# Kernel optimization log

Hardware: AMD Instinct MI355X
Metric: run time of the kernel (lower is better)

Reference implementation:

```python
import jax, jax.numpy as jnp
import numpy as np

D_MODEL = 384
D_STATE = 16
D_CONV = 4
EXPAND = 2
D_INNER = EXPAND * D_MODEL
DT_RANK = max(1, -(-D_MODEL // 16))  # ceil(d_model/16) = 24
BATCH = 32
SEQ = 1024


def _ssm_params(keys, prefix):
    s = 0.02
    n = lambda k, shp: jax.random.normal(k, shp, dtype=jnp.float32) * s
    A_log = jnp.broadcast_to(jnp.log(jnp.arange(1, D_STATE + 1, dtype=jnp.float32))[None, :], (D_INNER, D_STATE))
    return {
        prefix + '_in_w': n(keys[0], (2 * D_INNER, D_MODEL)),
        prefix + '_conv_w': n(keys[1], (D_INNER, 1, D_CONV)),
        prefix + '_conv_b': jnp.zeros((D_INNER,), jnp.float32),
        prefix + '_x_proj_w': n(keys[2], (DT_RANK + 2 * D_STATE, D_INNER)),
        prefix + '_dt_w': n(keys[3], (D_INNER, DT_RANK)),
        prefix + '_dt_b': jnp.zeros((D_INNER,), jnp.float32),
        prefix + '_A_log': A_log,
        prefix + '_D': jnp.ones((D_INNER,), jnp.float32),
        prefix + '_out_w': n(keys[4], (D_MODEL, D_INNER)),
    }


def setup_inputs() -> dict:
    key = jax.random.key(0)
    ks = jax.random.split(key, 13)
    inp = {
        'x': jax.random.normal(ks[0], (BATCH, SEQ, D_MODEL), dtype=jnp.float32),
        'ln_gamma': jnp.ones((D_MODEL,), jnp.float32),
        'ln_beta': jnp.zeros((D_MODEL,), jnp.float32),
        'gate_w': jax.random.normal(ks[11], (D_MODEL, 2 * D_MODEL), dtype=jnp.float32) * 0.02,
        'gate_b': jnp.zeros((D_MODEL,), jnp.float32),
    }
    inp.update(_ssm_params(ks[1:6], 'f'))
    inp.update(_ssm_params(ks[6:11], 'b'))
    return inp


def _selective_scan(xc, dt, A, Bm, Cm):
    # xc, dt: (B, L, d_inner); Bm, Cm: (B, L, N); A: (d_inner, N)
    h0 = jnp.zeros((xc.shape[0], xc.shape[2], A.shape[1]), xc.dtype)

    def step(h, inputs):
        x_t, dt_t, B_t, C_t = inputs          # (B,di), (B,di), (B,N), (B,N)
        dA = jnp.exp(dt_t[..., None] * A)     # (B, di, N)
        h = dA * h + (dt_t * x_t)[..., None] * B_t[:, None, :]
        y = jnp.einsum('bdn,bn->bd', h, C_t)
        return h, y

    xs = (jnp.moveaxis(xc, 1, 0), jnp.moveaxis(dt, 1, 0),
          jnp.moveaxis(Bm, 1, 0), jnp.moveaxis(Cm, 1, 0))
    _, ys = jax.lax.scan(step, h0, xs)
    return jnp.moveaxis(ys, 0, 1)  # (B, L, d_inner)


def _ssm(x, in_w, conv_w, conv_b, x_proj_w, dt_w, dt_b, A_log, Dp, out_w):
    L = x.shape[1]
    xz = jnp.einsum('bld,ed->ble', x, in_w)           # (B, L, 2*d_inner)
    xi, z = jnp.split(xz, 2, axis=-1)
    # depthwise causal conv1d (torch pads d_conv-1 then truncates to L)
    xc = jax.lax.conv_general_dilated(
        jnp.swapaxes(xi, 1, 2), conv_w, window_strides=(1,),
        padding=[(D_CONV - 1, 0)], feature_group_count=D_INNER,
        dimension_numbers=('NCH', 'OIH', 'NCH')) + conv_b[None, :, None]
    xc = jax.nn.silu(jnp.swapaxes(xc, 1, 2))          # (B, L, d_inner)
    xp = jnp.einsum('bld,ed->ble', xc, x_proj_w)      # (B, L, dt_rank+2N)
    dt = jax.nn.softplus(jnp.einsum('blr,dr->bld', xp[..., :DT_RANK], dt_w) + dt_b)
    Bm = xp[..., DT_RANK:DT_RANK + D_STATE]
    Cm = xp[..., DT_RANK + D_STATE:]
    A = -jnp.exp(A_log)
    y = _selective_scan(xc, dt, A, Bm, Cm)
    y = y + xc * Dp
    y = y * jax.nn.silu(z)
    return jnp.einsum('ble,de->bld', y, out_w)


def reference(x, ln_gamma, ln_beta,
              f_in_w, f_conv_w, f_conv_b, f_x_proj_w, f_dt_w, f_dt_b, f_A_log, f_D, f_out_w,
              b_in_w, b_conv_w, b_conv_b, b_x_proj_w, b_dt_w, b_dt_b, b_A_log, b_D, b_out_w,
              gate_w, gate_b):
    residual = x
    mu = jnp.mean(x, axis=-1, keepdims=True)
    var = jnp.mean((x - mu) ** 2, axis=-1, keepdims=True)
    xn = (x - mu) * jax.lax.rsqrt(var + 1e-5) * ln_gamma + ln_beta
    y_fwd = _ssm(xn, f_in_w, f_conv_w, f_conv_b, f_x_proj_w, f_dt_w, f_dt_b, f_A_log, f_D, f_out_w)
    y_bwd = _ssm(jnp.flip(xn, axis=1), b_in_w, b_conv_w, b_conv_b, b_x_proj_w, b_dt_w, b_dt_b, b_A_log, b_D, b_out_w)
    y_bwd = jnp.flip(y_bwd, axis=1)
    combined = jnp.concatenate([y_fwd, y_bwd], axis=-1)
    gate = jax.nn.sigmoid(jnp.einsum('blc,dc->bld', combined, gate_w) + gate_b)
    y = gate * y_fwd + (1.0 - gate) * y_bwd
    return y + residual
```

## Files before the change

### kernel.cpp

```cpp
#include <hip/hip_runtime.h>
#include <hip/hip_bf16.h>

#define BATCH  32
#define SEQ    1024
#define DMODEL 384
#define DINNER 768
#define DSTATE 16
#define DTRANK 24
#define NTOK   (BATCH * SEQ)
#define TC     32
#define CL     (SEQ / TC)
#define DTR_R  32

typedef __hip_bfloat16 bf16;
typedef __attribute__((ext_vector_type(8))) short frag_ab;
typedef __attribute__((ext_vector_type(4))) float frag_cd;

__device__ __forceinline__ float b2f(bf16 v) { return __bfloat162float(v); }
__device__ __forceinline__ bf16  f2b(float v) { return __float2bfloat16(v); }
__device__ __forceinline__ float ldx(const void* p, size_t i, bool f32m) {
    return f32m ? ((const float*)p)[i] : b2f(((const bf16*)p)[i]);
}

__device__ __forceinline__ void gld16(void* l, const void* g) {
    __builtin_amdgcn_global_load_lds(
        (const __attribute__((address_space(1))) unsigned int*)g,
        (__attribute__((address_space(3))) unsigned int*)l, 16, 0, 0);
}

__device__ __forceinline__ uint4 bmul8(uint4 y, uint4 s) {
    const bf16* yb = (const bf16*)&y;
    const bf16* sb = (const bf16*)&s;
    uint4 r;
    bf16* rb = (bf16*)&r;
#pragma unroll
    for (int j = 0; j < 8; ++j) rb[j] = f2b(b2f(yb[j]) * b2f(sb[j]));
    return r;
}

__global__ void detect_kernel(const unsigned short* __restrict__ x, int* flag) {
    int bad = 0;
    for (int i = threadIdx.x; i < 16384; i += 256) {
        int e = (x[i] >> 7) & 0xFF;
        bad |= (e >= 0xE0);
    }
    if (bad) atomicOr(flag, 1);
}

__global__ void struct_check(const float* __restrict__ alog, int* flag) {
    int c = blockIdx.x * 256 + threadIdx.x;
    if (c >= DINNER) return;
    float a0 = __expf(alog[c * 16]);
    int bad = 0;
#pragma unroll
    for (int n = 1; n < DSTATE; ++n) {
        float r = __expf(alog[c * 16 + n]) / a0;
        bad |= (fabsf(r - (float)(n + 1)) > 1e-3f * (n + 1));
    }
    if (bad) atomicOr(flag + 1, 1);
}

struct CvtF { const void* src[15]; float* dst[15]; int n[15]; };
struct CvtB { const void* src[7];  bf16*  dst[7];  int n[7];  };

__global__ void convert_f_kernel(CvtF p, const int* __restrict__ flag) {
    bool f32m = (*flag != 0);
    int y = blockIdx.y;
    const void* s = p.src[y];
    float* d = p.dst[y];
    int n = p.n[y];
    for (int i = blockIdx.x * 256 + threadIdx.x; i < n; i += gridDim.x * 256)
        d[i] = ldx(s, i, f32m);
}
__global__ void convert_b_kernel(CvtB p, const int* __restrict__ flag) {
    bool f32m = (*flag != 0);
    int y = blockIdx.y;
    const void* s = p.src[y];
    bf16* d = p.dst[y];
    int n = p.n[y];
    for (int i = blockIdx.x * 256 + threadIdx.x; i < n; i += gridDim.x * 256)
        d[i] = f2b(ldx(s, i, f32m));
}

__global__ void transpose_dtw(const float* __restrict__ w, float* __restrict__ wt) {
    int i = blockIdx.x * 256 + threadIdx.x;
    if (i >= DINNER * DTRANK) return;
    int c = i / DTRANK, r = i % DTRANK;
    wt[r * DINNER + c] = w[i];
}

__global__ void ln_kernel(const void* __restrict__ x, size_t xoff,
                          const float* __restrict__ gamma, const float* __restrict__ beta,
                          bf16* __restrict__ xn, const int* __restrict__ flag) {
    bool f32m = (*flag != 0);
    int wave = threadIdx.x >> 6;
    int lane = threadIdx.x & 63;
    int row  = blockIdx.x * 4 + wave;
    size_t base = xoff + (size_t)row * DMODEL;
    float v[6];
    float s = 0.f, s2 = 0.f;
#pragma unroll
    for (int i = 0; i < 6; ++i) {
        v[i] = ldx(x, base + lane + i * 64, f32m);
        s += v[i];
        s2 += v[i] * v[i];
    }
#pragma unroll
    for (int off = 32; off >= 1; off >>= 1) {
        s  += __shfl_down(s, off, 64);
        s2 += __shfl_down(s2, off, 64);
    }
    s  = __shfl(s, 0, 64);
    s2 = __shfl(s2, 0, 64);
    float mu   = s / DMODEL;
    float var  = s2 / DMODEL - mu * mu;
    float rstd = rsqrtf(var + 1e-5f);
    bf16* xnr = xn + (size_t)row * DMODEL;
#pragma unroll
    for (int i = 0; i < 6; ++i)
        xnr[lane + i * 64] = f2b((v[i] - mu) * rstd * gamma[lane + i * 64] + beta[lane + i * 64]);
}

__device__ __forceinline__ void compute_tile(const bf16 (*Al)[32], const bf16 (*Bl)[32],
                                             frag_cd acc[4][4], int wm, int wn,
                                             int mr, int quad) {
    frag_ab af[4], bfr[4];
#pragma unroll
    for (int r = 0; r < 4; ++r)
        af[r] = *(const frag_ab*)&Al[wm * 64 + r * 16 + mr][quad * 8];
#pragma unroll
    for (int c = 0; c < 4; ++c)
        bfr[c] = *(const frag_ab*)&Bl[wn * 64 + c * 16 + mr][quad * 8];
#pragma unroll
    for (int r = 0; r < 4; ++r)
#pragma unroll
        for (int c = 0; c < 4; ++c)
            acc[r][c] = __builtin_amdgcn_mfma_f32_16x16x32_bf16(af[r], bfr[c], acc[r][c], 0, 0, 0);
}

template <int MODE>
__global__ __launch_bounds__(256) void gemm_mfma(
    const bf16* __restrict__ A, const bf16* __restrict__ W,
    int K, int lda, int ldw, int nNT,
    bf16* __restrict__ C, int ldc, int cofs,
    float* __restrict__ Cf, bf16* __restrict__ Cz, const bf16* __restrict__ Sz,
    const float* __restrict__ gb, const void* __restrict__ xg, size_t xoff,
    void* __restrict__ outg, const int* __restrict__ flag) {
    __shared__ bf16 Als[2][128][32];
    __shared__ bf16 Bls[2][128][32];
    int tid = threadIdx.x;
    int lane = tid & 63;
    int w = tid >> 6;
    int wm = w & 1, wn = w >> 1;
    int wgid = blockIdx.x;
    int mt_lo = wgid & 7;
    int rr_ = wgid >> 3;
    int nt = rr_ % nNT;
    int mt = (rr_ / nNT) * 8 + mt_lo;
    int m0 = mt * 128, n0 = nt * 128;
    int row = tid >> 2, kc = tid & 3;
    int mr = lane & 15, quad = lane >> 4;

    const bf16* Ab0 = A + (size_t)(m0 + row) * lda + kc * 8;
    const bf16* Ab1 = A + (size_t)(m0 + 64 + row) * lda + kc * 8;
    const bf16* Wb0 = W + (size_t)(n0 + row) * ldw + kc * 8;
    const bf16* Wb1 = W + (size_t)(n0 + 64 + row) * ldw + kc * 8;
    const bf16* Zb0 = (MODE == 5) ? (Sz + (size_t)(m0 + row) * DINNER + kc * 8) : nullptr;
    const bf16* Zb1 = (MODE == 5) ? (Sz + (size_t)(m0 + 64 + row) * DINNER + kc * 8) : nullptr;

    frag_cd acc[4][4] = {};
    const int NT = K / 32;

    if (MODE == 5) {
        uint4 eya0, eya1, esz0, esz1;
        uint4 oya0, oya1, osz0, osz1;
        eya0 = *(const uint4*)(Ab0);      eya1 = *(const uint4*)(Ab1);
        esz0 = *(const uint4*)(Zb0);      esz1 = *(const uint4*)(Zb1);
        oya0 = *(const uint4*)(Ab0 + 32); oya1 = *(const uint4*)(Ab1 + 32);
        osz0 = *(const uint4*)(Zb0 + 32); osz1 = *(const uint4*)(Zb1 + 32);
        *(uint4*)&Als[0][row][kc * 8]      = bmul8(eya0, esz0);
        *(uint4*)&Als[0][64 + row][kc * 8] = bmul8(eya1, esz1);
        gld16(&Bls[0][row][kc * 8], Wb0);
        gld16(&Bls[0][64 + row][kc * 8], Wb1);
        __syncthreads();
        for (int t = 0; t < NT; t += 2) {
            int k1 = (t + 1) * 32, k2 = (t + 2) * 32, k3 = (t + 3) * 32;
            *(uint4*)&Als[1][row][kc * 8]      = bmul8(oya0, osz0);
            *(uint4*)&Als[1][64 + row][kc * 8] = bmul8(oya1, osz1);
            gld16(&Bls[1][row][kc * 8], Wb0 + k1);
            gld16(&Bls[1][64 + row][kc * 8], Wb1 + k1);
            if (t + 2 < NT) {
                eya0 = *(const uint4*)(Ab0 + k2); eya1 = *(const uint4*)(Ab1 + k2);
                esz0 = *(const uint4*)(Zb0 + k2); esz1 = *(const uint4*)(Zb1 + k2);
            }
            compute_tile(Als[0], Bls[0], acc, wm, wn, mr, quad);
            __syncthreads();
            if (t + 2 < NT) {
                *(uint4*)&Als[0][row][kc * 8]      = bmul8(eya0, esz0);
                *(uint4*)&Als[0][64 + row][kc * 8] = bmul8(eya1, esz1);
                gld16(&Bls[0][row][kc * 8], Wb0 + k2);
                gld16(&Bls[0][64 + row][kc * 8], Wb1 + k2);
                oya0 = *(const uint4*)(Ab0 + k3); oya1 = *(const uint4*)(Ab1 + k3);
                osz0 = *(const uint4*)(Zb0 + k3); osz1 = *(const uint4*)(Zb1 + k3);
            }
            compute_tile(Als[1], Bls[1], acc, wm, wn, mr, quad);
            __syncthreads();
        }
    } else {
        gld16(&Als[0][row][kc * 8], Ab0);
        gld16(&Als[0][64 + row][kc * 8], Ab1);
        gld16(&Bls[0][row][kc * 8], Wb0);
        gld16(&Bls[0][64 + row][kc * 8], Wb1);
        __syncthreads();
        for (int t = 0; t < NT; t += 2) {
            int k1 = (t + 1) * 32, k2 = (t + 2) * 32;
            gld16(&Als[1][row][kc * 8], Ab0 + k1);
            gld16(&Als[1][64 + row][kc * 8], Ab1 + k1);
            gld16(&Bls[1][row][kc * 8], Wb0 + k1);
            gld16(&Bls[1][64 + row][kc * 8], Wb1 + k1);
            compute_tile(Als[0], Bls[0], acc, wm, wn, mr, quad);
            __syncthreads();
            if (t + 2 < NT) {
                gld16(&Als[0][row][kc * 8], Ab0 + k2);
                gld16(&Als[0][64 + row][kc * 8], Ab1 + k2);
                gld16(&Bls[0][row][kc * 8], Wb0 + k2);
                gld16(&Bls[0][64 + row][kc * 8], Wb1 + k2);
            }
            compute_tile(Als[1], Bls[1], acc, wm, wn, mr, quad);
            __syncthreads();
        }
    }

    bool f32m = (MODE == 1) ? (*flag != 0) : false;
#pragma unroll
    for (int r = 0; r < 4; ++r) {
#pragma unroll
        for (int c = 0; c < 4; ++c) {
#pragma unroll
            for (int reg = 0; reg < 4; ++reg) {
                int gm = m0 + wm * 64 + r * 16 + quad * 4 + reg;
                int gn = n0 + wn * 64 + c * 16 + mr;
                float v = acc[r][c][reg];
                if (MODE == 0 || MODE == 5) {
                    C[(size_t)gm * ldc + cofs + gn] = f2b(v);
                } else if (MODE == 2) {
                    if (gn < DTRANK + 2 * DSTATE) Cf[(size_t)gm * 56 + gn] = v;
                } else if (MODE == 4) {
                    if (gn < DINNER) {
                        C[(size_t)gm * DINNER + gn] = f2b(v);
                    } else {
                        float sz = v / (1.f + __expf(-v));
                        Cz[(size_t)gm * DINNER + (gn - DINNER)] = f2b(sz);
                    }
                } else {
                    float g   = 1.f / (1.f + __expf(-(v + gb[gn])));
                    float yfv = b2f(A[(size_t)gm * DINNER + gn]);
                    float ybv = b2f(A[(size_t)gm * DINNER + DMODEL + gn]);
                    size_t gi = xoff + (size_t)gm * DMODEL + gn;
                    float xv  = f32m ? ((const float*)xg)[gi] : b2f(((const bf16*)xg)[gi]);
                    float rr  = g * yfv + (1.f - g) * ybv + xv;
                    if (f32m) ((float*)outg)[gi] = rr;
                    else      ((bf16*)outg)[gi]  = f2b(rr);
                }
            }
        }
    }
}

__global__ void conv_kernel(const bf16* __restrict__ xi_buf, const float* __restrict__ cw,
                            const float* __restrict__ cb, bf16* __restrict__ xc, int reverse) {
    int g = blockIdx.x * blockDim.x + threadIdx.x;
    int c8 = (g % (DINNER / 8)) * 8;
    int bl = g / (DINNER / 8);
    int l = bl % SEQ;
    int b = bl / SEQ;
    float4 wq[8];
#pragma unroll
    for (int j = 0; j < 8; ++j) wq[j] = *(const float4*)(cw + (c8 + j) * 4);
    float4 cb0 = *(const float4*)(cb + c8);
    float4 cb1 = *(const float4*)(cb + c8 + 4);
    float acc[8] = {cb0.x, cb0.y, cb0.z, cb0.w, cb1.x, cb1.y, cb1.z, cb1.w};

    const bf16* base = xi_buf + (size_t)b * SEQ * DINNER + c8;
#pragma unroll
    for (int k = 0; k < 4; ++k) {
        int ll = reverse ? (l + k) : (l - 3 + k);
        int wk = reverse ? (3 - k) : k;
        if (ll >= 0 && ll < SEQ) {
            uint4 v = *(const uint4*)(base + (size_t)ll * DINNER);
            const bf16* vb = (const bf16*)&v;
#pragma unroll
            for (int j = 0; j < 8; ++j)
                acc[j] += b2f(vb[j]) * ((const float*)&wq[j])[wk];
        }
    }
    uint4 out;
    bf16* ob = (bf16*)&out;
#pragma unroll
    for (int j = 0; j < 8; ++j)
        ob[j] = f2b(acc[j] / (1.f + __expf(-acc[j])));
    *(uint4*)(xc + (size_t)bl * DINNER + c8) = out;
}

__global__ __launch_bounds__(256, 4) void dt_kernel(const float* __restrict__ xp,
                                                    const float* __restrict__ dtwT,
                                                    const float* __restrict__ dtb,
                                                    float* __restrict__ dtf) {
    __shared__ float4 xps[DTR_R][6];
    int tid = threadIdx.x;
    int c = blockIdx.y * 256 + tid;
    float w[DTRANK];
#pragma unroll
    for (int r = 0; r < DTRANK; ++r) w[r] = dtwT[r * DINNER + c];
#pragma unroll
    for (int r = 0; r < DTRANK; ++r) asm volatile("" : "+v"(w[r]));
    float bias = dtb[c];

    size_t row0 = (size_t)blockIdx.x * DTR_R;
    for (int i = tid; i < DTR_R * 6; i += 256) {
        int s = i / 6, q = i % 6;
        xps[s][q] = *(const float4*)(xp + (row0 + s) * 56 + q * 4);
    }
    __syncthreads();

    for (int s = 0; s < DTR_R; s += 2) {
        float a0 = bias, a1 = bias;
#pragma unroll
        for (int q = 0; q < 6; ++q) {
            float4 x0 = xps[s][q];
            float4 x1 = xps[s + 1][q];
            a0 += x0.x * w[q * 4 + 0];  a1 += x1.x * w[q * 4 + 0];
            a0 += x0.y * w[q * 4 + 1];  a1 += x1.y * w[q * 4 + 1];
            a0 += x0.z * w[q * 4 + 2];  a1 += x1.z * w[q * 4 + 2];
            a0 += x0.w * w[q * 4 + 3];  a1 += x1.w * w[q * 4 + 3];
        }
        float e0 = __builtin_amdgcn_exp2f(fabsf(a0) * -1.44269504f);
        float e1 = __builtin_amdgcn_exp2f(fabsf(a1) * -1.44269504f);
        a0 = fmaxf(a0, 0.f) + 0.69314718f * __builtin_amdgcn_logf(1.f + e0);
        a1 = fmaxf(a1, 0.f) + 0.69314718f * __builtin_amdgcn_logf(1.f + e1);
        dtf[(row0 + s) * DINNER + c]     = a0;
        dtf[(row0 + s + 1) * DINNER + c] = a1;
    }
}

template <int PHASE>
__global__ void scan_phase(const float* __restrict__ xp, const bf16* __restrict__ xc,
                           const float* __restrict__ dtf, const float* __restrict__ Alog,
                           const float* __restrict__ Dg, float* __restrict__ states,
                           bf16* __restrict__ ydir, int reverse, const int* __restrict__ flag) {
    __shared__ float xps[16][32];
    bool generic = (flag[1] != 0);
    int tid = threadIdx.x;
    int bidx = blockIdx.x;
    int tc  = bidx % TC;
    int cgb = bidx / TC;
    int cg  = cgb % 6;
    int bb  = cgb / 6;
    int c = cg * 128 + tid;

    float Av0 = -__expf(Alog[c * DSTATE]);
    float Av[DSTATE];
    if (generic) {
#pragma unroll
        for (int n = 0; n < DSTATE; ++n) Av[n] = -__expf(Alog[c * DSTATE + n]);
    }
    float Dv = Dg[c];

    float h[DSTATE];
    float Q = 1.f, Pg[DSTATE];
    size_t sbase = (size_t)bidx * 32;
    if (PHASE == 0) {
#pragma unroll
        for (int n = 0; n < DSTATE; ++n) { h[n] = 0.f; Pg[n] = 1.f; }
    } else {
#pragma unroll
        for (int n = 0; n < DSTATE; ++n) h[n] = states[(sbase + n) * 128 + tid];
    }

    const size_t brow = (size_t)bb * SEQ;
    const int t0 = tc * CL;
    const int tr0 = reverse ? (SEQ - 1 - t0) : t0;
    const long dstep = reverse ? -(long)DINNER : (long)DINNER;
    const float* pdt = dtf + (brow + tr0) * DINNER + c;
    const bf16*  pxc = xc  + (brow + tr0) * DINNER + c;
    bf16* pyd = (PHASE == 1) ? (ydir + (brow + tr0) * DINNER + c) : nullptr;

    for (int g0 = 0; g0 < CL; g0 += 16) {
        __syncthreads();
        for (int i = tid; i < 16 * 32; i += 128) {
            int s = i >> 5, r = i & 31;
            int t = t0 + g0 + s;
            int tr = reverse ? (SEQ - 1 - t) : t;
            xps[s][r] = xp[(brow + tr) * 56 + 24 + r];
        }
        __syncthreads();
        for (int s = 0; s < 16; ++s) {
            float dt  = *pdt;  pdt += dstep;
            float xcv = b2f(*pxc);  pxc += dstep;
            float dtx = dt * xcv;
            float accv = 0.f;
            if (!generic) {
                float e1 = __expf(dt * Av0);
                float d = e1;
#pragma unroll
                for (int n = 0; n < DSTATE; ++n) {
                    h[n] = d * h[n] + dtx * xps[s][n];
                    if (PHASE == 1) accv += h[n] * xps[s][16 + n];
                    d *= e1;
                }
                if (PHASE == 0) Q *= e1;
            } else {
#pragma unroll
                for (int n = 0; n < DSTATE; ++n) {
                    float dA = __expf(dt * Av[n]);
                    h[n] = dA * h[n] + dtx * xps[s][n];
                    if (PHASE == 0) Pg[n] *= dA;
                    else accv += h[n] * xps[s][16 + n];
                }
            }
            if (PHASE == 1) {
                *pyd = f2b(accv + xcv * Dv);
                pyd += dstep;
            }
        }
    }
    if (PHASE == 0) {
        if (!generic) {
            float d = Q;
#pragma unroll
            for (int n = 0; n < DSTATE; ++n) { Pg[n] = d; d *= Q; }
        }
#pragma unroll
        for (int n = 0; n < DSTATE; ++n) {
            states[(sbase + n) * 128 + tid]      = Pg[n];
            states[(sbase + 16 + n) * 128 + tid] = h[n];
        }
    }
}

__global__ void scan_stitch(float* __restrict__ states) {
    int tid = threadIdx.x;
    int cgb = blockIdx.x;
    float h[DSTATE];
#pragma unroll
    for (int n = 0; n < DSTATE; ++n) h[n] = 0.f;
    for (int tc = 0; tc < TC; ++tc) {
        size_t base = ((size_t)cgb * TC + tc) * 32;
#pragma unroll
        for (int n = 0; n < DSTATE; ++n) {
            float Pv = states[(base + n) * 128 + tid];
            float ev = states[(base + 16 + n) * 128 + tid];
            states[(base + n) * 128 + tid] = h[n];
            h[n] = Pv * h[n] + ev;
        }
    }
}

extern "C" void kernel_launch(void* const* d_in, const int* in_sizes, int n_in,
                              void* d_out, int out_size, void* d_ws, size_t ws_size,
                              hipStream_t stream) {
    (void)n_in; (void)out_size;
    bool dict_order = (in_sizes[4] < 2048);
    int fbase = dict_order ? 5 : 3;
    int bbase = dict_order ? 14 : 12;
    int gwi = dict_order ? 3 : 21;
    int gbi = dict_order ? 4 : 22;

    auto al = [](size_t b) { return (b + 255) & ~(size_t)255; };
    char* ws = (char*)d_ws;
    size_t off = 0;
    auto alloc = [&](size_t bytes) {
        void* p = ws + off;
        off += al(bytes);
        return p;
    };

    int* flag = (int*)alloc(256);

    CvtF pf{};
    int cf = 0;
    auto addf = [&](int idx, int n) {
        float* d = (float*)alloc((size_t)n * 4);
        pf.src[cf] = d_in[idx]; pf.dst[cf] = d; pf.n[cf] = n; ++cf;
        return d;
    };
    float* ln_gc   = addf(1, DMODEL);
    float* ln_bc   = addf(2, DMODEL);
    float* gate_bc = addf(gbi, DMODEL);
    float* convw_f[2], *convb_f[2], *dtw_f[2], *dtb_f[2], *alog_f[2], *dd_f[2];
    for (int d = 0; d < 2; ++d) {
        int base = d ? bbase : fbase;
        convw_f[d] = addf(base + 1, DINNER * 4);
        convb_f[d] = addf(base + 2, DINNER);
        dtw_f[d]   = addf(base + 4, DINNER * DTRANK);
        dtb_f[d]   = addf(base + 5, DINNER);
        alog_f[d]  = addf(base + 6, DINNER * DSTATE);
        dd_f[d]    = addf(base + 7, DINNER);
    }

    CvtB pb{};
    int cb = 0;
    auto addb = [&](int idx, int n, size_t alloc_n) {
        bf16* d = (bf16*)alloc(alloc_n * 2);
        pb.src[cb] = d_in[idx]; pb.dst[cb] = d; pb.n[cb] = n; ++cb;
        return d;
    };
    bf16* gate_wb = addb(gwi, DMODEL * 2 * DMODEL, (size_t)DMODEL * 2 * DMODEL);
    bf16 *inw_b[2], *xpw_b[2], *outw_b[2];
    for (int d = 0; d < 2; ++d) {
        int base = d ? bbase : fbase;
        inw_b[d]  = addb(base + 0, 2 * DINNER * DMODEL, (size_t)2 * DINNER * DMODEL);
        xpw_b[d]  = addb(base + 3, 56 * DINNER, (size_t)128 * DINNER);
        outw_b[d] = addb(base + 8, DMODEL * DINNER, (size_t)DMODEL * DINNER);
    }

    float* dtwT_f[2];
    for (int d = 0; d < 2; ++d)
        dtwT_f[d] = (float*)alloc((size_t)DTRANK * DINNER * 4);

    size_t fixed = off;

    auto chunk_need = [&](int bc) {
        size_t T = (size_t)bc * SEQ;
        return al(T * DMODEL * 2)
             + 2 * al(T * DINNER * 2)
             + al(T * 56 * 4)
             + al(T * DINNER * 4)
             + al(T * DINNER * 2)
             + al(T * DINNER * 2)
             + al((size_t)bc * 6 * TC * 32 * 128 * 4);
    };
    int Bc = 32;
    while (Bc > 1 && fixed + chunk_need(Bc) > ws_size) Bc >>= 1;
    size_t T = (size_t)Bc * SEQ;
    int nMT = (int)(T / 128);

    bf16*  xn_c   = (bf16*)alloc(T * DMODEL * 2);
    bf16*  xib    = (bf16*)alloc(T * DINNER * 2);
    bf16*  xcb    = (bf16*)alloc(T * DINNER * 2);
    float* xpb    = (float*)alloc(T * 56 * 4);
    float* dtfb   = (float*)alloc(T * DINNER * 4);
    bf16*  zbb    = (bf16*)alloc(T * DINNER * 2);
    bf16*  ycat   = (bf16*)alloc(T * DINNER * 2);
    float* states = (float*)alloc((size_t)Bc * 6 * TC * 32 * 128 * 4);
    bf16*  ydir   = xib;

    hipMemsetAsync(flag, 0, 8, stream);
    for (int d = 0; d < 2; ++d)
        hipMemsetAsync(xpw_b[d], 0, (size_t)128 * DINNER * 2, stream);
    detect_kernel<<<1, 256, 0, stream>>>((const unsigned short*)d_in[0], flag);
    convert_f_kernel<<<dim3(8, 15), 256, 0, stream>>>(pf, flag);
    convert_b_kernel<<<dim3(32, 7), 256, 0, stream>>>(pb, flag);
    struct_check<<<3, 256, 0, stream>>>(alog_f[0], flag);
    struct_check<<<3, 256, 0, stream>>>(alog_f[1], flag);
    for (int d = 0; d < 2; ++d)
        transpose_dtw<<<(DINNER * DTRANK + 255) / 256, 256, 0, stream>>>(dtw_f[d], dtwT_f[d]);

    for (int c0 = 0; c0 < BATCH; c0 += Bc) {
        size_t tok0 = (size_t)c0 * SEQ;

        ln_kernel<<<(unsigned)(T / 4), 256, 0, stream>>>(
            d_in[0], tok0 * DMODEL, ln_gc, ln_bc, xn_c, flag);

        for (int dir = 0; dir < 2; ++dir) {
            gemm_mfma<4><<<nMT * 12, 256, 0, stream>>>(
                xn_c, inw_b[dir], DMODEL, DMODEL, DMODEL, 12,
                xib, DINNER, 0, nullptr, zbb, nullptr,
                nullptr, nullptr, 0, nullptr, flag);
            conv_kernel<<<(unsigned)((T * DINNER) / 2048), 256, 0, stream>>>(
                xib, convw_f[dir], convb_f[dir], xcb, dir);
            gemm_mfma<2><<<nMT * 1, 256, 0, stream>>>(
                xcb, xpw_b[dir], DINNER, DINNER, DINNER, 1,
                nullptr, 0, 0, xpb, nullptr, nullptr,
                nullptr, nullptr, 0, nullptr, flag);
            dt_kernel<<<dim3((unsigned)(T / DTR_R), 3), 256, 0, stream>>>(
                xpb, dtwT_f[dir], dtb_f[dir], dtfb);
            scan_phase<0><<<Bc * 6 * TC, 128, 0, stream>>>(
                xpb, xcb, dtfb, alog_f[dir], dd_f[dir], states, nullptr, dir, flag);
            scan_stitch<<<Bc * 6, 128, 0, stream>>>(states);
            scan_phase<1><<<Bc * 6 * TC, 128, 0, stream>>>(
                xpb, xcb, dtfb, alog_f[dir], dd_f[dir], states, ydir, dir, flag);
            gemm_mfma<5><<<nMT * 3, 256, 0, stream>>>(
                ydir, outw_b[dir], DINNER, DINNER, DINNER, 3,
                ycat, DINNER, dir * DMODEL, nullptr, nullptr, zbb,
                nullptr, nullptr, 0, nullptr, flag);
        }

        gemm_mfma<1><<<nMT * 3, 256, 0, stream>>>(
            ycat, gate_wb, DINNER, DINNER, DINNER, 3,
            nullptr, 0, 0, nullptr, nullptr, nullptr,
            gate_bc, d_in[0], tok0 * DMODEL, d_out, flag);
    }
}
```

Measured before the change: 1.266 ms.

## Split scan state dimension across two half-waves per channel

Each channel's 16 SSM states are now split across two lanes (8 states each), with the lane pair joined through a cross-lane shuffle to combine the output sum. Channel groups shrink from 128 to 64 per block, so block count doubles and per-thread register use and the serial dependency chain shrink. The aim is more parallelism and latency hiding in the sequential scan. In exchange, the per-step dt/xc loads are duplicated across both halves, a shuffle is added per step, and the state buffer layout and the stitch kernel are changed to match.

```diff
diff --git a/kernel.cpp b/kernel.cpp
--- a/kernel.cpp
+++ b/kernel.cpp
@@ -344,37 +344,44 @@
 }
 
 template <int PHASE>
-__global__ void scan_phase(const float* __restrict__ xp, const bf16* __restrict__ xc,
-                           const float* __restrict__ dtf, const float* __restrict__ Alog,
-                           const float* __restrict__ Dg, float* __restrict__ states,
-                           bf16* __restrict__ ydir, int reverse, const int* __restrict__ flag) {
+__global__ __launch_bounds__(128) void scan_phase(
+        const float* __restrict__ xp, const bf16* __restrict__ xc,
+        const float* __restrict__ dtf, const float* __restrict__ Alog,
+        const float* __restrict__ Dg, float* __restrict__ states,
+        bf16* __restrict__ ydir, int reverse, const int* __restrict__ flag) {
     __shared__ float xps[16][32];
     bool generic = (flag[1] != 0);
     int tid = threadIdx.x;
     int bidx = blockIdx.x;
     int tc  = bidx % TC;
     int cgb = bidx / TC;
-    int cg  = cgb % 6;
-    int bb  = cgb / 6;
-    int c = cg * 128 + tid;
+    int cg  = cgb % 12;
+    int bb  = cgb / 12;
+    int wave = tid >> 6;
+    int lane = tid & 63;
+    int half = lane >> 5;
+    int lch  = lane & 31;
+    int wch  = wave * 32 + lch;
+    int c  = cg * 64 + wch;
+    int ns = half * 8;
 
     float Av0 = -__expf(Alog[c * DSTATE]);
-    float Av[DSTATE];
+    float Av[8];
     if (generic) {
 #pragma unroll
-        for (int n = 0; n < DSTATE; ++n) Av[n] = -__expf(Alog[c * DSTATE + n]);
+        for (int j = 0; j < 8; ++j) Av[j] = -__expf(Alog[c * DSTATE + ns + j]);
     }
     float Dv = Dg[c];
 
-    float h[DSTATE];
-    float Q = 1.f, Pg[DSTATE];
+    float h[8];
+    float Q = 1.f, Pg[8];
     size_t sbase = (size_t)bidx * 32;
     if (PHASE == 0) {
 #pragma unroll
-        for (int n = 0; n < DSTATE; ++n) { h[n] = 0.f; Pg[n] = 1.f; }
+        for (int j = 0; j < 8; ++j) { h[j] = 0.f; Pg[j] = 1.f; }
     } else {
 #pragma unroll
-        for (int n = 0; n < DSTATE; ++n) h[n] = states[(sbase + n) * 128 + tid];
+        for (int j = 0; j < 8; ++j) h[j] = states[(sbase + ns + j) * 64 + wch];
     }
 
     const size_t brow = (size_t)bb * SEQ;
@@ -401,39 +408,52 @@
             float accv = 0.f;
             if (!generic) {
                 float e1 = __expf(dt * Av0);
-                float d = e1;
-#pragma unroll
-                for (int n = 0; n < DSTATE; ++n) {
-                    h[n] = d * h[n] + dtx * xps[s][n];
-                    if (PHASE == 1) accv += h[n] * xps[s][16 + n];
+                float d;
+                if (half) {
+                    float e2 = e1 * e1, e4 = e2 * e2, e8 = e4 * e4;
+                    d = e8 * e1;
+                } else {
+                    d = e1;
+                }
+#pragma unroll
+                for (int j = 0; j < 8; ++j) {
+                    h[j] = d * h[j] + dtx * xps[s][ns + j];
+                    if (PHASE == 1) accv += h[j] * xps[s][16 + ns + j];
                     d *= e1;
                 }
                 if (PHASE == 0) Q *= e1;
             } else {
 #pragma unroll
-                for (int n = 0; n < DSTATE; ++n) {
-                    float dA = __expf(dt * Av[n]);
-                    h[n] = dA * h[n] + dtx * xps[s][n];
-                    if (PHASE == 0) Pg[n] *= dA;
-                    else accv += h[n] * xps[s][16 + n];
+                for (int j = 0; j < 8; ++j) {
+                    float dA = __expf(dt * Av[j]);
+                    h[j] = dA * h[j] + dtx * xps[s][ns + j];
+                    if (PHASE == 0) Pg[j] *= dA;
+                    else accv += h[j] * xps[s][16 + ns + j];
                 }
             }
             if (PHASE == 1) {
-                *pyd = f2b(accv + xcv * Dv);
+                accv += __shfl_xor(accv, 32, 64);
+                if (!half) *pyd = f2b(accv + xcv * Dv);
                 pyd += dstep;
             }
         }
     }
     if (PHASE == 0) {
         if (!generic) {
-            float d = Q;
-#pragma unroll
-            for (int n = 0; n < DSTATE; ++n) { Pg[n] = d; d *= Q; }
-        }
-#pragma unroll
-        for (int n = 0; n < DSTATE; ++n) {
-            states[(sbase + n) * 128 + tid]      = Pg[n];
-            states[(sbase + 16 + n) * 128 + tid] = h[n];
+            float d;
+            if (half) {
+                float q2 = Q * Q, q4 = q2 * q2, q8 = q4 * q4;
+                d = q8 * Q;
+            } else {
+                d = Q;
+            }
+#pragma unroll
+            for (int j = 0; j < 8; ++j) { Pg[j] = d; d *= Q; }
+        }
+#pragma unroll
+        for (int j = 0; j < 8; ++j) {
+            states[(sbase + ns + j) * 64 + wch]      = Pg[j];
+            states[(sbase + 16 + ns + j) * 64 + wch] = h[j];
         }
     }
 }
@@ -441,17 +461,19 @@
 __global__ void scan_stitch(float* __restrict__ states) {
     int tid = threadIdx.x;
     int cgb = blockIdx.x;
-    float h[DSTATE];
-#pragma unroll
-    for (int n = 0; n < DSTATE; ++n) h[n] = 0.f;
+    int wch = tid & 63;
+    int ns  = (tid >> 6) * 8;
+    float h[8];
+#pragma unroll
+    for (int j = 0; j < 8; ++j) h[j] = 0.f;
     for (int tc = 0; tc < TC; ++tc) {
         size_t base = ((size_t)cgb * TC + tc) * 32;
 #pragma unroll
-        for (int n = 0; n < DSTATE; ++n) {
-            float Pv = states[(base + n) * 128 + tid];
-            float ev = states[(base + 16 + n) * 128 + tid];
-            states[(base + n) * 128 + tid] = h[n];
-            h[n] = Pv * h[n] + ev;
+        for (int j = 0; j < 8; ++j) {
+            float Pv = states[(base + ns + j) * 64 + wch];
+            float ev = states[(base + 16 + ns + j) * 64 + wch];
+            states[(base + ns + j) * 64 + wch] = h[j];
+            h[j] = Pv * h[j] + ev;
         }
     }
 }
@@ -528,7 +550,7 @@
              + al(T * DINNER * 4)
              + al(T * DINNER * 2)
              + al(T * DINNER * 2)
-             + al((size_t)bc * 6 * TC * 32 * 128 * 4);
+             + al((size_t)bc * 12 * TC * 32 * 64 * 4);
     };
     int Bc = 32;
     while (Bc > 1 && fixed + chunk_need(Bc) > ws_size) Bc >>= 1;
@@ -542,7 +564,7 @@
     float* dtfb   = (float*)alloc(T * DINNER * 4);
     bf16*  zbb    = (bf16*)alloc(T * DINNER * 2);
     bf16*  ycat   = (bf16*)alloc(T * DINNER * 2);
-    float* states = (float*)alloc((size_t)Bc * 6 * TC * 32 * 128 * 4);
+    float* states = (float*)alloc((size_t)Bc * 12 * TC * 32 * 64 * 4);
     bf16*  ydir   = xib;
 
     hipMemsetAsync(flag, 0, 8, stream);
@@ -575,10 +597,10 @@
                 nullptr, nullptr, 0, nullptr, flag);
             dt_kernel<<<dim3((unsigned)(T / DTR_R), 3), 256, 0, stream>>>(
                 xpb, dtwT_f[dir], dtb_f[dir], dtfb);
-            scan_phase<0><<<Bc * 6 * TC, 128, 0, stream>>>(
+            scan_phase<0><<<Bc * 12 * TC, 128, 0, stream>>>(
                 xpb, xcb, dtfb, alog_f[dir], dd_f[dir], states, nullptr, dir, flag);
-            scan_stitch<<<Bc * 6, 128, 0, stream>>>(states);
-            scan_phase<1><<<Bc * 6 * TC, 128, 0, stream>>>(
+            scan_stitch<<<Bc * 12, 128, 0, stream>>>(states);
+            scan_phase<1><<<Bc * 12 * TC, 128, 0, stream>>>(
                 xpb, xcb, dtfb, alog_f[dir], dd_f[dir], states, ydir, dir, flag);
             gemm_mfma<5><<<nMT * 3, 256, 0, stream>>>(
                 ydir, outw_b[dir], DINNER, DINNER, DINNER, 3,
```

New measurement: 1.265 ms. About the same (-0.0%).
